# Kernel tuning notes

Measured on AMD Instinct MI355X. Metric: run time of the kernel, lower is better.

Reference implementation:

```python
import jax, jax.numpy as jnp
import numpy as np

N, E, D, L = 40000, 640000, 128, 4

def setup_inputs() -> dict:
    key = jax.random.key(0)
    ks = jax.random.split(key, 4)
    x = jax.random.normal(ks[0], (N, D), dtype=jnp.float32)
    edge_index = jax.random.randint(ks[1], (2, E), 0, N)
    edge_weight = jax.random.uniform(ks[2], (E,), dtype=jnp.float32)
    W = jax.random.normal(ks[3], (L, D, D), dtype=jnp.float32) / np.float32(np.sqrt(D))
    b = jnp.zeros((L, D), jnp.float32)
    gamma = jnp.ones((L, D), jnp.float32)
    beta = jnp.zeros((L, D), jnp.float32)
    return dict(x=x, edge_index=edge_index, edge_weight=edge_weight, W=W, b=b, gamma=gamma, beta=beta)

def _gcn_norm(edge_index, edge_weight, n):
    # PyG gcn_norm: add self loops (weight 1), symmetric D^-1/2 A D^-1/2
    loops = jnp.arange(n)
    src = jnp.concatenate([edge_index[0], loops])
    dst = jnp.concatenate([edge_index[1], loops])
    ew = jnp.concatenate([edge_weight, jnp.ones((n,), edge_weight.dtype)])
    deg = jax.ops.segment_sum(ew, dst, num_segments=n)
    dis = jnp.where(deg > 0, jax.lax.rsqrt(jnp.maximum(deg, 1e-12)), 0.0)
    return src, dst, dis[src] * ew * dis[dst]

def _batchnorm(h, g, bta):
    # training-mode BatchNorm1d over the node axis, biased variance, eps=1e-5
    mu = h.mean(0)
    var = h.var(0)
    return g * (h - mu) * jax.lax.rsqrt(var + 1e-5) + bta

def reference(x, edge_index, edge_weight, W, b, gamma, beta):
    n = x.shape[0]
    n_layers = W.shape[0]
    src, dst, norm = _gcn_norm(edge_index, edge_weight, n)
    x0 = x  # decoded_reshaped_x for skip connections
    for i in range(n_layers):
        h = x @ W[i]                                   # [N, D] linear (GCNConv.lin)
        msg = h[src] * norm[:, None]                   # gather + scale, [E+N, D]
        h = jax.ops.segment_sum(msg, dst, num_segments=n) + b[i]
        if i < n_layers - 1:
            h = jax.nn.relu(h)
        h = h + x0                                     # skip connection
        if i != n_layers - 2:
            h = _batchnorm(h, gamma[i], beta[i])
        x = h
    return x
```

## Files before the change

### kernel.cpp

```cpp
#include <hip/hip_runtime.h>
#include <cstdint>
#include <cstddef>

constexpr int N = 40000;
constexpr int E = 640000;
constexpr int D = 128;
constexpr int NBKT = 157;
constexpr int BCAP = 5120;
constexpr int AGG_GRID = 2500;

typedef _Float16 half8 __attribute__((ext_vector_type(8)));
typedef float f32x4 __attribute__((ext_vector_type(4)));
typedef unsigned long long ull;

__device__ __forceinline__ unsigned int pack_rec(int idx, float v) {
  union { _Float16 h; unsigned short us; } c; c.h = (_Float16)v;
  return (unsigned int)idx | ((unsigned int)c.us << 16);
}


__global__ void k_zero(uint4* __restrict__ p) {
  int i = blockIdx.x * 256 + threadIdx.x;
  if (i < 2136) p[i] = make_uint4(0u, 0u, 0u, 0u);
}


__global__ void k_bigprep(const int* __restrict__ ei, const float* __restrict__ ew,
                          const float* __restrict__ X, _Float16* __restrict__ Xh,
                          const float* __restrict__ W, _Float16* __restrict__ Wt,
                          ull* __restrict__ binned, int* __restrict__ bktcnt) {
  int bid = blockIdx.x, t = threadIdx.x;
  if (bid < NBKT) {
    __shared__ int lhist[NBKT], lbase[NBKT], lrank[NBKT];
    if (t < NBKT) { lhist[t] = 0; lrank[t] = 0; }
    __syncthreads();
    int e16 = bid * 256 + t;
    bool act = (e16 < E / 16);
    int4 s4[4], d4[4]; float4 w4[4];
    if (act) {
#pragma unroll
      for (int u = 0; u < 4; ++u) {
        s4[u] = ((const int4*)ei)[e16 * 4 + u];
        d4[u] = ((const int4*)(ei + E))[e16 * 4 + u];
        w4[u] = ((const float4*)ew)[e16 * 4 + u];
      }
#pragma unroll
      for (int u = 0; u < 4; ++u) {
        atomicAdd(&lhist[d4[u].x >> 8], 1); atomicAdd(&lhist[d4[u].y >> 8], 1);
        atomicAdd(&lhist[d4[u].z >> 8], 1); atomicAdd(&lhist[d4[u].w >> 8], 1);
      }
    }
    __syncthreads();
    if (t < NBKT && lhist[t] > 0) lbase[t] = atomicAdd(&bktcnt[t], lhist[t]);
    __syncthreads();
    if (act) {
      auto emit = [&](int s, int dcol, float w) {
        int bkt = dcol >> 8;
        int rank = atomicAdd(&lrank[bkt], 1);
        int pos = lbase[bkt] + rank;
        ull rec = (ull)(unsigned)(s & 0xFFFF)
                | ((ull)(unsigned)(dcol & 255) << 16)
                | ((ull)__float2uint_rn(w * 67108864.0f) << 24);
        if (pos < BCAP) binned[(size_t)bkt * BCAP + pos] = rec;
      };
#pragma unroll
      for (int u = 0; u < 4; ++u) {
        emit(s4[u].x, d4[u].x, w4[u].x); emit(s4[u].y, d4[u].y, w4[u].y);
        emit(s4[u].z, d4[u].z, w4[u].z); emit(s4[u].w, d4[u].w, w4[u].w);
      }
    }
  } else if (bid < 2657) {
    int i = (bid - NBKT) * 256 + t;
    float4 v0 = ((const float4*)X)[i * 2];
    float4 v1 = ((const float4*)X)[i * 2 + 1];
    half8 h;
    h[0] = (_Float16)v0.x; h[1] = (_Float16)v0.y; h[2] = (_Float16)v0.z; h[3] = (_Float16)v0.w;
    h[4] = (_Float16)v1.x; h[5] = (_Float16)v1.y; h[6] = (_Float16)v1.z; h[7] = (_Float16)v1.w;
    ((half8*)Xh)[i] = h;
  } else {
    int o = (bid - 2657) * 256 + t;
    int l = o >> 14, rem = o & 16383, c = rem >> 7, k = rem & 127;
    Wt[o] = (_Float16)W[l * 16384 + k * 128 + c];
  }
}


__global__ __launch_bounds__(256) void k_bstats(const ull* __restrict__ binned,
    const int* __restrict__ bktcnt, float* __restrict__ dis, int* __restrict__ rowc,
    int* __restrict__ bsum, int* __restrict__ hist, int* __restrict__ bpre,
    int* __restrict__ histcur, unsigned int* __restrict__ done) {
  __shared__ ull acc[256];
  __shared__ int lhist[64];
  __shared__ int red[256];
  __shared__ int amlast;
  int bkt = blockIdx.x, t = threadIdx.x;
  acc[t] = 0ULL;
  if (t < 64) lhist[t] = 0;
  __syncthreads();
  int cnt = min(bktcnt[bkt], BCAP);
  const ull* bp = binned + (size_t)bkt * BCAP;
  for (int e = t; e < cnt; e += 256) {
    ull r = bp[e];
    int local = (int)((r >> 16) & 255);
    atomicAdd(&acc[local], (1ULL << 40) | (r >> 24));
  }
  __syncthreads();
  int row = bkt * 256 + t;
  int c = 0;
  if (row < N) {
    ull a = acc[t];
    c = (int)(a >> 40) + 1;
    float deg = (float)(a & ((1ULL << 40) - 1)) * (1.0f / 67108864.0f);
    dis[row] = rsqrtf(deg + 1.0f);
    rowc[row] = c;
    atomicAdd(&lhist[min(c, 63)], 1);
  }
  red[t] = c;
  __syncthreads();
  for (int off = 128; off > 0; off >>= 1) {
    if (t < off) red[t] += red[t + off];
    __syncthreads();
  }
  if (t == 0) bsum[bkt] = red[0];
  if (t < 64 && lhist[t] > 0) atomicAdd(&hist[t], lhist[t]);
  __syncthreads();
  if (t == 0) {
    __threadfence();
    amlast = (atomicAdd(done, 1u) == NBKT - 1);
  }
  __syncthreads();
  if (!amlast) return;
  __threadfence();
  red[t] = (t < NBKT) ? bsum[t] : 0;
  __syncthreads();
  for (int off = 1; off < 256; off <<= 1) {
    int v = red[t];
    int add = (t >= off) ? red[t - off] : 0;
    __syncthreads();
    red[t] = v + add;
    __syncthreads();
  }
  if (t < NBKT) bpre[t] = (t == 0) ? 0 : red[t - 1];
  if (t < 64) {
    int s = 0;
    for (int b2 = t + 1; b2 < 64; ++b2) s += hist[b2];
    histcur[t] = s;
  }
}


__device__ __forceinline__ void gemm_body(int bid, int tid, const _Float16* __restrict__ X,
    const _Float16* __restrict__ Wt, const float* __restrict__ sums,
    const float* __restrict__ gamma, const float* __restrict__ beta, int useBN,
    const float* __restrict__ dis, _Float16* __restrict__ Hout,
    float* scl, float* shf) {
  if (tid < 128) {
    if (useBN) {
      float s = 0.f, s2 = 0.f;
#pragma unroll
      for (int r = 0; r < 8; ++r) { s += sums[r * 256 + tid]; s2 += sums[r * 256 + 128 + tid]; }
      float mu = s * (1.0f / N);
      float var = s2 * (1.0f / N) - mu * mu;
      float rs = rsqrtf(var + 1e-5f);
      float sc = gamma[tid] * rs;
      scl[tid] = sc;
      shf[tid] = beta[tid] - mu * sc;
    } else {
      scl[tid] = 1.0f;
      shf[tid] = 0.0f;
    }
  }
  __syncthreads();

  int wv = tid >> 6, lane = tid & 63;
  int fr = lane & 15, kg = lane >> 4;
  int arow = bid * 64 + wv * 16 + fr;
  const _Float16* xrow = X + (size_t)arow * D;

  half8 af[4];
#pragma unroll
  for (int kc = 0; kc < 4; ++kc) {
    int k0 = kc * 32 + kg * 8;
    half8 xr = *(const half8*)&xrow[k0];
    half8 a;
#pragma unroll
    for (int u = 0; u < 8; ++u)
      a[u] = (_Float16)fmaf((float)xr[u], scl[k0 + u], shf[k0 + u]);
    af[kc] = a;
  }

  f32x4 acc[8];
#pragma unroll
  for (int ct = 0; ct < 8; ++ct) acc[ct] = (f32x4){0.f, 0.f, 0.f, 0.f};

#pragma unroll
  for (int ct = 0; ct < 8; ++ct) {
    const _Float16* wcol = Wt + (size_t)(ct * 16 + fr) * 128;
#pragma unroll
    for (int kc = 0; kc < 4; ++kc) {
      half8 bf = *(const half8*)&wcol[kc * 32 + kg * 8];
      acc[ct] = __builtin_amdgcn_mfma_f32_16x16x32_f16(af[kc], bf, acc[ct], 0, 0, 0);
    }
  }

  int orow0 = bid * 64 + wv * 16 + kg * 4;
#pragma unroll
  for (int rg = 0; rg < 4; ++rg) {
    int grow = orow0 + rg;
    float dsv = dis[grow];
    _Float16* hrow = Hout + (size_t)grow * D;
#pragma unroll
    for (int ct = 0; ct < 8; ++ct)
      hrow[ct * 16 + fr] = (_Float16)(acc[ct][rg] * dsv);
  }
}

__global__ __launch_bounds__(256) void k_gemm(const _Float16* __restrict__ X,
    const _Float16* __restrict__ Wt, const float* __restrict__ sums,
    const float* __restrict__ gamma, const float* __restrict__ beta, int useBN,
    const float* __restrict__ dis, _Float16* __restrict__ Hout) {
  __shared__ float scl[128], shf[128];
  gemm_body(blockIdx.x, threadIdx.x, X, Wt, sums, gamma, beta, useBN, dis, Hout, scl, shf);
}


__global__ __launch_bounds__(256) void k_gemm0_fill(const _Float16* __restrict__ X,
    const _Float16* __restrict__ Wt, const float* __restrict__ dis,
    _Float16* __restrict__ Hout,
    const int* __restrict__ rowc, const int* __restrict__ bpre,
    const ull* __restrict__ binned, const int* __restrict__ bktcnt,
    unsigned int* __restrict__ cv, int* __restrict__ offs,
    int* __restrict__ histcur, int* __restrict__ perm) {
  int bid = blockIdx.x, t = threadIdx.x;
  if (bid < 625) {
    __shared__ float scl[128], shf[128];
    gemm_body(bid, t, X, Wt, (const float*)nullptr, (const float*)nullptr,
              (const float*)nullptr, 0, dis, Hout, scl, shf);
  } else if (bid < 625 + NBKT) {
    int bkt = bid - 625;
    __shared__ int lcur[256];
    __shared__ int s[256];
    int row = bkt * 256 + t;
    int c = (row < N) ? rowc[row] : 0;
    s[t] = c;
    __syncthreads();
    for (int off = 1; off < 256; off <<= 1) {
      int v = s[t];
      int add = (t >= off) ? s[t - off] : 0;
      __syncthreads();
      s[t] = v + add;
      __syncthreads();
    }
    int run = bpre[bkt] + s[t] - c;
    if (row < N) {
      offs[row] = run;
      cv[run] = pack_rec(row, 1.0f);
      lcur[t] = run + 1;
    } else {
      lcur[t] = 0;
    }
    if (row == N - 1) offs[N] = N + E;
    __syncthreads();
    int cnt = min(bktcnt[bkt], BCAP);
    const ull* bp = binned + (size_t)bkt * BCAP;
    for (int e = t; e < cnt; e += 256) {
      ull r = bp[e];
      int local = (int)((r >> 16) & 255);
      int srcv = (int)(r & 0xFFFFu);
      float w = (float)(unsigned)(r >> 24) * (1.0f / 67108864.0f);
      int slot = atomicAdd(&lcur[local], 1);
      cv[slot] = pack_rec(srcv, w);
    }
  } else {
    __shared__ int lhist[64], lbase[64];
    if (t < 64) lhist[t] = 0;
    __syncthreads();
    int i = (bid - (625 + NBKT)) * 256 + t;
    bool valid = (i < N);
    int bin = 0, myrank = 0;
    if (valid) {
      int c = rowc[i];
      bin = min(c, 63);
      myrank = atomicAdd(&lhist[bin], 1);
    }
    __syncthreads();
    if (t < 64 && lhist[t] > 0) lbase[t] = atomicAdd(&histcur[t], lhist[t]);
    __syncthreads();
    if (valid) perm[lbase[bin] + myrank] = i;
  }
}


__global__ __launch_bounds__(256) void k_agg(const uint4* __restrict__ Hu4,
    const int* __restrict__ offs, const unsigned int* __restrict__ cv,
    const float* __restrict__ dis, const float* __restrict__ bias,
    const uint4* __restrict__ x0h, const int* __restrict__ perm,
    int doRelu, int doStats, int outF32,
    _Float16* __restrict__ Hout16, float* __restrict__ Houtf, float* __restrict__ sums) {
  int t = threadIdx.x;
  int sl = t & 15;
  int g = t >> 4;
  int row = perm[blockIdx.x * 16 + g];
  float4 bv0 = ((const float4*)bias)[sl * 2];
  float4 bv1 = ((const float4*)bias)[sl * 2 + 1];
  const uint4* hp = Hu4 + sl;

  int e0 = offs[row], e1 = offs[row + 1];
  float a[8];
#pragma unroll
  for (int k = 0; k < 8; ++k) a[k] = 0.f;
  for (int eb = e0; eb < e1; eb += 16) {
    int m = min(16, e1 - eb);
    unsigned int rec = 0;
    if (sl < m) rec = cv[eb + sl];
#pragma unroll 1
    for (int g8 = 0; g8 < 2; ++g8) {
      int b0 = g8 * 8;
      if (b0 >= m) break;
      uint4 cu[8]; float vv[8];
#pragma unroll
      for (int j = 0; j < 8; ++j) {
        int jj = b0 + j;
        int jc = (jj < m) ? jj : (m - 1);
        unsigned int rj = __shfl(rec, jc, 16);
        union { unsigned short us; _Float16 h; } vh; vh.us = (unsigned short)(rj >> 16);
        vv[j] = (jj < m) ? (float)vh.h : 0.f;
        cu[j] = hp[(size_t)(rj & 0xFFFFu) * 16];
      }
#pragma unroll
      for (int j = 0; j < 8; ++j) {
        union { uint4 u; _Float16 hh[8]; } c8; c8.u = cu[j];
#pragma unroll
        for (int k = 0; k < 8; ++k) a[k] = fmaf((float)c8.hh[k], vv[j], a[k]);
      }
    }
  }
  float dr = dis[row];
  union { uint4 u; _Float16 hh[8]; } xc;
  xc.u = x0h[(size_t)row * 16 + sl];
  float rr[8];
  rr[0] = fmaf(a[0], dr, bv0.x); rr[1] = fmaf(a[1], dr, bv0.y);
  rr[2] = fmaf(a[2], dr, bv0.z); rr[3] = fmaf(a[3], dr, bv0.w);
  rr[4] = fmaf(a[4], dr, bv1.x); rr[5] = fmaf(a[5], dr, bv1.y);
  rr[6] = fmaf(a[6], dr, bv1.z); rr[7] = fmaf(a[7], dr, bv1.w);
  if (doRelu) {
#pragma unroll
    for (int k = 0; k < 8; ++k) rr[k] = fmaxf(rr[k], 0.f);
  }
#pragma unroll
  for (int k = 0; k < 8; ++k) rr[k] += (float)xc.hh[k];
  if (outF32) {
    float4 o0, o1;
    o0.x = rr[0]; o0.y = rr[1]; o0.z = rr[2]; o0.w = rr[3];
    o1.x = rr[4]; o1.y = rr[5]; o1.z = rr[6]; o1.w = rr[7];
    ((float4*)Houtf)[(size_t)row * 32 + sl * 2] = o0;
    ((float4*)Houtf)[(size_t)row * 32 + sl * 2 + 1] = o1;
  } else {
    union { uint4 u; _Float16 hh[8]; } ov;
#pragma unroll
    for (int k = 0; k < 8; ++k) ov.hh[k] = (_Float16)rr[k];
    ((uint4*)Hout16)[(size_t)row * 16 + sl] = ov.u;
  }

  if (doStats) {
    __shared__ float reds[16 * 128], reds2[16 * 128];
#pragma unroll
    for (int k = 0; k < 8; ++k) {
      reds[g * 128 + sl * 8 + k] = rr[k];
      reds2[g * 128 + sl * 8 + k] = rr[k] * rr[k];
    }
    __syncthreads();
    if (t < 128) {
      float ts = 0.f, ts2 = 0.f;
#pragma unroll
      for (int j = 0; j < 16; ++j) { ts += reds[j * 128 + t]; ts2 += reds2[j * 128 + t]; }
      int rep = blockIdx.x & 7;
      atomicAdd(&sums[rep * 256 + t], ts);
      atomicAdd(&sums[rep * 256 + 128 + t], ts2);
    }
  }
}


__global__ __launch_bounds__(256) void k_bnapply(float* __restrict__ H,
    const float* __restrict__ sums, const float* __restrict__ gamma,
    const float* __restrict__ beta) {
  __shared__ float scl[128], shf[128];
  int t = threadIdx.x;
  if (t < 128) {
    float s = 0.f, s2 = 0.f;
#pragma unroll
    for (int r = 0; r < 8; ++r) { s += sums[r * 256 + t]; s2 += sums[r * 256 + 128 + t]; }
    float mu = s * (1.0f / N);
    float var = s2 * (1.0f / N) - mu * mu;
    float rs = rsqrtf(var + 1e-5f);
    float sc = gamma[t] * rs;
    scl[t] = sc;
    shf[t] = beta[t] - mu * sc;
  }
  __syncthreads();
  size_t i = (size_t)blockIdx.x * 256 + t;
  float4 v = ((const float4*)H)[i];
  int c = (int)(i & 31) * 4;
  v.x = fmaf(v.x, scl[c + 0], shf[c + 0]);
  v.y = fmaf(v.y, scl[c + 1], shf[c + 1]);
  v.z = fmaf(v.z, scl[c + 2], shf[c + 2]);
  v.w = fmaf(v.w, scl[c + 3], shf[c + 3]);
  ((float4*)H)[i] = v;
}


extern "C" void kernel_launch(void* const* d_in, const int* in_sizes, int n_in,
                              void* d_out, int out_size, void* d_ws, size_t ws_size,
                              hipStream_t stream) {
  const float* x     = (const float*)d_in[0];
  const int*   ei    = (const int*)d_in[1];
  const float* ew    = (const float*)d_in[2];
  const float* W     = (const float*)d_in[3];
  const float* b     = (const float*)d_in[4];
  const float* gamma = (const float*)d_in[5];
  const float* beta  = (const float*)d_in[6];
  float* out = (float*)d_out;

  char* ws = (char*)d_ws;
  _Float16* hlin   = (_Float16*)ws;
  _Float16* hagg16 = (_Float16*)(ws + 10240000);
  _Float16* xh     = (_Float16*)(ws + 20480000);
  float* sums4    = (float*)(ws + 30720000);
  int*   hist     = (int*)  (ws + 30752768);
  int*   histcur  = (int*)  (ws + 30753024);
  int*   bktcnt   = (int*)  (ws + 30753280);
  unsigned int* done = (unsigned int*)(ws + 30753920);
  float* dis      = (float*)(ws + 30754176);
  int*   offs     = (int*)  (ws + 30914176);
  int*   rowc     = (int*)  (ws + 31074192);
  unsigned int* cv= (unsigned int*)(ws + 31234192);
  int*   perm     = (int*)  (ws + 33954192);
  int*   bsum     = (int*)  (ws + 34114192);
  int*   bpre     = (int*)  (ws + 34114832);
  _Float16* Wt    = (_Float16*)(ws + 34115472);
  ull* binned     = (ull*)  (ws + 34246544);

  k_zero<<<9, 256, 0, stream>>>((uint4*)sums4);
  k_bigprep<<<2913, 256, 0, stream>>>(ei, ew, x, xh, W, Wt, binned, bktcnt);
  k_bstats<<<NBKT, 256, 0, stream>>>(binned, bktcnt, dis, rowc, bsum, hist,
                                     bpre, histcur, done);

  for (int l = 0; l < 4; ++l) {
    const _Float16* xin = (l == 0) ? xh : hagg16;
    if (l == 0) {
      k_gemm0_fill<<<625 + NBKT + 157, 256, 0, stream>>>(xin, Wt, dis, hlin,
                                                         rowc, bpre, binned, bktcnt,
                                                         cv, offs, histcur, perm);
    } else {
      int useBN = (l == 1 || l == 2) ? 1 : 0;
      const float* sprev = sums4 + (size_t)(l - 1) * 2048;
      k_gemm<<<N / 64, 256, 0, stream>>>(xin, Wt + (size_t)l * 16384, sprev,
                                         gamma + (size_t)(l - 1) * D,
                                         beta + (size_t)(l - 1) * D, useBN, dis, hlin);
    }
    int doStats = (l != 2) ? 1 : 0;
    int doRelu = (l < 3) ? 1 : 0;
    int outF32 = (l == 3) ? 1 : 0;
    k_agg<<<AGG_GRID, 256, 0, stream>>>((const uint4*)hlin, offs, cv, dis,
                                        b + (size_t)l * D, (const uint4*)xh, perm,
                                        doRelu, doStats, outF32, hagg16, out,
                                        sums4 + (size_t)l * 2048);
  }
  k_bnapply<<<(N * D / 4) / 256, 256, 0, stream>>>(out, sums4 + 3 * 2048,
                                                   gamma + 3 * D, beta + 3 * D);
}
```

Baseline: 230.5 us.

## Slice feature columns into four planes so aggregation gathers stay cache-resident

Stores the fp16 node features as four column slices of 32 channels each, with the GEMM reading and writing that sliced layout. The aggregation kernel runs four times as many blocks, one set per slice, and each thread gathers a 4-byte pair instead of a 16-byte chunk. The aim is to shrink the working set of each gather pass (40000×32 fp16 per slice) so random neighbour reads hit in L2 or infinity cache. In exchange, CSR edge records are re-read once per slice, each gather moves less data, and nontemporal hints are added on the streaming loads and stores.

```diff
diff --git a/kernel.cpp b/kernel.cpp
--- a/kernel.cpp
+++ b/kernel.cpp
@@ -8,9 +8,15 @@
 constexpr int NBKT = 157;
 constexpr int BCAP = 5120;
 constexpr int AGG_GRID = 2500;
+constexpr int NSLICE = 4;
+constexpr size_t SLICE_H  = (size_t)N * 32;
+constexpr size_t SLICE_D  = (size_t)N * 16;
+constexpr size_t SLICE_H8 = (size_t)N * 4;
 
 typedef _Float16 half8 __attribute__((ext_vector_type(8)));
+typedef _Float16 half2v __attribute__((ext_vector_type(2)));
 typedef float f32x4 __attribute__((ext_vector_type(4)));
+typedef float f32x2 __attribute__((ext_vector_type(2)));
 typedef unsigned long long ull;
 
 __device__ __forceinline__ unsigned int pack_rec(int idx, float v) {
@@ -76,7 +82,8 @@
     half8 h;
     h[0] = (_Float16)v0.x; h[1] = (_Float16)v0.y; h[2] = (_Float16)v0.z; h[3] = (_Float16)v0.w;
     h[4] = (_Float16)v1.x; h[5] = (_Float16)v1.y; h[6] = (_Float16)v1.z; h[7] = (_Float16)v1.w;
-    ((half8*)Xh)[i] = h;
+    int r = i >> 4, c8 = i & 15;
+    ((half8*)Xh)[(size_t)(c8 >> 2) * SLICE_H8 + (size_t)r * 4 + (c8 & 3)] = h;
   } else {
     int o = (bid - 2657) * 256 + t;
     int l = o >> 14, rem = o & 16383, c = rem >> 7, k = rem & 127;
@@ -175,13 +182,12 @@
   int wv = tid >> 6, lane = tid & 63;
   int fr = lane & 15, kg = lane >> 4;
   int arow = bid * 64 + wv * 16 + fr;
-  const _Float16* xrow = X + (size_t)arow * D;
 
   half8 af[4];
 #pragma unroll
   for (int kc = 0; kc < 4; ++kc) {
     int k0 = kc * 32 + kg * 8;
-    half8 xr = *(const half8*)&xrow[k0];
+    half8 xr = *(const half8*)&X[(size_t)kc * SLICE_H + (size_t)arow * 32 + kg * 8];
     half8 a;
 #pragma unroll
     for (int u = 0; u < 8; ++u)
@@ -208,10 +214,11 @@
   for (int rg = 0; rg < 4; ++rg) {
     int grow = orow0 + rg;
     float dsv = dis[grow];
-    _Float16* hrow = Hout + (size_t)grow * D;
-#pragma unroll
-    for (int ct = 0; ct < 8; ++ct)
-      hrow[ct * 16 + fr] = (_Float16)(acc[ct][rg] * dsv);
+#pragma unroll
+    for (int ct = 0; ct < 8; ++ct) {
+      Hout[(size_t)(ct >> 1) * SLICE_H + (size_t)grow * 32 + (ct & 1) * 16 + fr] =
+          (_Float16)(acc[ct][rg] * dsv);
+    }
   }
 }
 
@@ -291,92 +298,72 @@
 }
 
 
-__global__ __launch_bounds__(256) void k_agg(const uint4* __restrict__ Hu4,
+__global__ __launch_bounds__(256) void k_agg(const unsigned int* __restrict__ Hu,
     const int* __restrict__ offs, const unsigned int* __restrict__ cv,
     const float* __restrict__ dis, const float* __restrict__ bias,
-    const uint4* __restrict__ x0h, const int* __restrict__ perm,
+    const unsigned int* __restrict__ x0u, const int* __restrict__ perm,
     int doRelu, int doStats, int outF32,
-    _Float16* __restrict__ Hout16, float* __restrict__ Houtf, float* __restrict__ sums) {
+    unsigned int* __restrict__ Hout16, float* __restrict__ Houtf,
+    float* __restrict__ sums) {
   int t = threadIdx.x;
+  int blk = blockIdx.x % AGG_GRID;
+  int slice = blockIdx.x / AGG_GRID;
   int sl = t & 15;
   int g = t >> 4;
-  int row = perm[blockIdx.x * 16 + g];
-  float4 bv0 = ((const float4*)bias)[sl * 2];
-  float4 bv1 = ((const float4*)bias)[sl * 2 + 1];
-  const uint4* hp = Hu4 + sl;
+  int row = perm[blk * 16 + g];
+  int C0 = slice * 32;
+  float bvx = bias[C0 + sl * 2];
+  float bvy = bias[C0 + sl * 2 + 1];
+  const unsigned int* hb = Hu + (size_t)slice * SLICE_D + sl;
 
   int e0 = offs[row], e1 = offs[row + 1];
-  float a[8];
-#pragma unroll
-  for (int k = 0; k < 8; ++k) a[k] = 0.f;
+  float a0 = 0.f, a1 = 0.f;
   for (int eb = e0; eb < e1; eb += 16) {
     int m = min(16, e1 - eb);
     unsigned int rec = 0;
-    if (sl < m) rec = cv[eb + sl];
-#pragma unroll 1
-    for (int g8 = 0; g8 < 2; ++g8) {
-      int b0 = g8 * 8;
-      if (b0 >= m) break;
-      uint4 cu[8]; float vv[8];
-#pragma unroll
-      for (int j = 0; j < 8; ++j) {
-        int jj = b0 + j;
-        int jc = (jj < m) ? jj : (m - 1);
-        unsigned int rj = __shfl(rec, jc, 16);
-        union { unsigned short us; _Float16 h; } vh; vh.us = (unsigned short)(rj >> 16);
-        vv[j] = (jj < m) ? (float)vh.h : 0.f;
-        cu[j] = hp[(size_t)(rj & 0xFFFFu) * 16];
-      }
-#pragma unroll
-      for (int j = 0; j < 8; ++j) {
-        union { uint4 u; _Float16 hh[8]; } c8; c8.u = cu[j];
-#pragma unroll
-        for (int k = 0; k < 8; ++k) a[k] = fmaf((float)c8.hh[k], vv[j], a[k]);
-      }
+    if (sl < m) rec = __builtin_nontemporal_load(&cv[eb + sl]);
+#pragma unroll 4
+    for (int j = 0; j < m; ++j) {
+      unsigned int rj = __shfl(rec, j, 16);
+      union { unsigned short us; _Float16 h; } vh; vh.us = (unsigned short)(rj >> 16);
+      float vj = (float)vh.h;
+      union { unsigned int u; half2v h; } hh;
+      hh.u = hb[(size_t)(rj & 0xFFFFu) * 16];
+      a0 = fmaf((float)hh.h[0], vj, a0);
+      a1 = fmaf((float)hh.h[1], vj, a1);
     }
   }
   float dr = dis[row];
-  union { uint4 u; _Float16 hh[8]; } xc;
-  xc.u = x0h[(size_t)row * 16 + sl];
-  float rr[8];
-  rr[0] = fmaf(a[0], dr, bv0.x); rr[1] = fmaf(a[1], dr, bv0.y);
-  rr[2] = fmaf(a[2], dr, bv0.z); rr[3] = fmaf(a[3], dr, bv0.w);
-  rr[4] = fmaf(a[4], dr, bv1.x); rr[5] = fmaf(a[5], dr, bv1.y);
-  rr[6] = fmaf(a[6], dr, bv1.z); rr[7] = fmaf(a[7], dr, bv1.w);
-  if (doRelu) {
-#pragma unroll
-    for (int k = 0; k < 8; ++k) rr[k] = fmaxf(rr[k], 0.f);
-  }
-#pragma unroll
-  for (int k = 0; k < 8; ++k) rr[k] += (float)xc.hh[k];
+  union { unsigned int u; half2v h; } xc;
+  xc.u = __builtin_nontemporal_load(&x0u[(size_t)slice * SLICE_D + (size_t)row * 16 + sl]);
+  float r0 = fmaf(a0, dr, bvx);
+  float r1 = fmaf(a1, dr, bvy);
+  if (doRelu) { r0 = fmaxf(r0, 0.f); r1 = fmaxf(r1, 0.f); }
+  r0 += (float)xc.h[0];
+  r1 += (float)xc.h[1];
   if (outF32) {
-    float4 o0, o1;
-    o0.x = rr[0]; o0.y = rr[1]; o0.z = rr[2]; o0.w = rr[3];
-    o1.x = rr[4]; o1.y = rr[5]; o1.z = rr[6]; o1.w = rr[7];
-    ((float4*)Houtf)[(size_t)row * 32 + sl * 2] = o0;
-    ((float4*)Houtf)[(size_t)row * 32 + sl * 2 + 1] = o1;
+    f32x2 o; o[0] = r0; o[1] = r1;
+    __builtin_nontemporal_store(o, (f32x2*)&Houtf[(size_t)row * 128 + C0 + sl * 2]);
   } else {
-    union { uint4 u; _Float16 hh[8]; } ov;
-#pragma unroll
-    for (int k = 0; k < 8; ++k) ov.hh[k] = (_Float16)rr[k];
-    ((uint4*)Hout16)[(size_t)row * 16 + sl] = ov.u;
+    union { unsigned int u; half2v h; } ov;
+    ov.h[0] = (_Float16)r0; ov.h[1] = (_Float16)r1;
+    Hout16[(size_t)slice * SLICE_D + (size_t)row * 16 + sl] = ov.u;
   }
 
   if (doStats) {
-    __shared__ float reds[16 * 128], reds2[16 * 128];
-#pragma unroll
-    for (int k = 0; k < 8; ++k) {
-      reds[g * 128 + sl * 8 + k] = rr[k];
-      reds2[g * 128 + sl * 8 + k] = rr[k] * rr[k];
-    }
-    __syncthreads();
-    if (t < 128) {
+    __shared__ float reds[512], reds2[512];
+    reds[g * 32 + sl * 2]      = r0;
+    reds[g * 32 + sl * 2 + 1]  = r1;
+    reds2[g * 32 + sl * 2]     = r0 * r0;
+    reds2[g * 32 + sl * 2 + 1] = r1 * r1;
+    __syncthreads();
+    if (t < 32) {
       float ts = 0.f, ts2 = 0.f;
 #pragma unroll
-      for (int j = 0; j < 16; ++j) { ts += reds[j * 128 + t]; ts2 += reds2[j * 128 + t]; }
-      int rep = blockIdx.x & 7;
-      atomicAdd(&sums[rep * 256 + t], ts);
-      atomicAdd(&sums[rep * 256 + 128 + t], ts2);
+      for (int q = 0; q < 16; ++q) { ts += reds[q * 32 + t]; ts2 += reds2[q * 32 + t]; }
+      int rep = blk & 7;
+      atomicAdd(&sums[rep * 256 + C0 + t], ts);
+      atomicAdd(&sums[rep * 256 + 128 + C0 + t], ts2);
     }
   }
 }
@@ -462,9 +449,11 @@
     int doStats = (l != 2) ? 1 : 0;
     int doRelu = (l < 3) ? 1 : 0;
     int outF32 = (l == 3) ? 1 : 0;
-    k_agg<<<AGG_GRID, 256, 0, stream>>>((const uint4*)hlin, offs, cv, dis,
-                                        b + (size_t)l * D, (const uint4*)xh, perm,
-                                        doRelu, doStats, outF32, hagg16, out,
+    k_agg<<<NSLICE * AGG_GRID, 256, 0, stream>>>((const unsigned int*)hlin, offs, cv,
+                                        dis, b + (size_t)l * D,
+                                        (const unsigned int*)xh, perm,
+                                        doRelu, doStats, outF32,
+                                        (unsigned int*)hagg16, out,
                                         sums4 + (size_t)l * 2048);
   }
   k_bnapply<<<(N * D / 4) / 256, 256, 0, stream>>>(out, sums4 + 3 * 2048,
```

Measured after the change: 342.5 us. 1.49x slower.

## Group each row's CSR edges by source-node tile and restructure gather loop

Applied to the files above, without the earlier changes.

Edges in each destination row are now ordered by one of four source-index tiles, with per-row tile counts packed into a 64-bit word built in the stats kernel and used by the fill kernel to lay out four sub-ranges per row. The aggregation kernel walks the tiles in order, aiming to improve L2 locality of the feature-row gathers. The gather loop also changes from batching eight independent loads before the FMAs to a simple per-edge load-and-accumulate loop, which may reduce memory-level parallelism. The extra tile counters add shared-memory atomics in preprocessing.

```diff
diff --git a/kernel.cpp b/kernel.cpp
--- a/kernel.cpp
+++ b/kernel.cpp
@@ -16,6 +16,10 @@
 __device__ __forceinline__ unsigned int pack_rec(int idx, float v) {
   union { _Float16 h; unsigned short us; } c; c.h = (_Float16)v;
   return (unsigned int)idx | ((unsigned int)c.us << 16);
+}
+
+__device__ __forceinline__ int src_tile(int s) {
+  return (int)(((unsigned)s * 6711u) >> 26);
 }
 
 
@@ -87,14 +91,17 @@
 
 __global__ __launch_bounds__(256) void k_bstats(const ull* __restrict__ binned,
     const int* __restrict__ bktcnt, float* __restrict__ dis, int* __restrict__ rowc,
+    ull* __restrict__ tilecnt,
     int* __restrict__ bsum, int* __restrict__ hist, int* __restrict__ bpre,
     int* __restrict__ histcur, unsigned int* __restrict__ done) {
   __shared__ ull acc[256];
+  __shared__ ull cnt4[256];
   __shared__ int lhist[64];
   __shared__ int red[256];
   __shared__ int amlast;
   int bkt = blockIdx.x, t = threadIdx.x;
   acc[t] = 0ULL;
+  cnt4[t] = 0ULL;
   if (t < 64) lhist[t] = 0;
   __syncthreads();
   int cnt = min(bktcnt[bkt], BCAP);
@@ -102,7 +109,9 @@
   for (int e = t; e < cnt; e += 256) {
     ull r = bp[e];
     int local = (int)((r >> 16) & 255);
+    int src = (int)(r & 0xFFFFu);
     atomicAdd(&acc[local], (1ULL << 40) | (r >> 24));
+    atomicAdd(&cnt4[local], 1ULL << (16 * src_tile(src)));
   }
   __syncthreads();
   int row = bkt * 256 + t;
@@ -113,6 +122,7 @@
     float deg = (float)(a & ((1ULL << 40) - 1)) * (1.0f / 67108864.0f);
     dis[row] = rsqrtf(deg + 1.0f);
     rowc[row] = c;
+    tilecnt[row] = cnt4[t] + (1ULL << (16 * src_tile(row)));
     atomicAdd(&lhist[min(c, 63)], 1);
   }
   red[t] = c;
@@ -227,7 +237,8 @@
 __global__ __launch_bounds__(256) void k_gemm0_fill(const _Float16* __restrict__ X,
     const _Float16* __restrict__ Wt, const float* __restrict__ dis,
     _Float16* __restrict__ Hout,
-    const int* __restrict__ rowc, const int* __restrict__ bpre,
+    const int* __restrict__ rowc, const ull* __restrict__ tilecnt,
+    const int* __restrict__ bpre,
     const ull* __restrict__ binned, const int* __restrict__ bktcnt,
     unsigned int* __restrict__ cv, int* __restrict__ offs,
     int* __restrict__ histcur, int* __restrict__ perm) {
@@ -238,7 +249,7 @@
               (const float*)nullptr, 0, dis, Hout, scl, shf);
   } else if (bid < 625 + NBKT) {
     int bkt = bid - 625;
-    __shared__ int lcur[256];
+    __shared__ int lcur[256 * 4];
     __shared__ int s[256];
     int row = bkt * 256 + t;
     int c = (row < N) ? rowc[row] : 0;
@@ -254,10 +265,20 @@
     int run = bpre[bkt] + s[t] - c;
     if (row < N) {
       offs[row] = run;
-      cv[run] = pack_rec(row, 1.0f);
-      lcur[t] = run + 1;
+      ull tc = tilecnt[row];
+      int b0 = run;
+      int b1 = b0 + (int)(tc & 0xFFFF);
+      int b2 = b1 + (int)((tc >> 16) & 0xFFFF);
+      int b3 = b2 + (int)((tc >> 32) & 0xFFFF);
+      lcur[t * 4 + 0] = b0; lcur[t * 4 + 1] = b1;
+      lcur[t * 4 + 2] = b2; lcur[t * 4 + 3] = b3;
+      int ts = src_tile(row);
+      int slot = lcur[t * 4 + ts];
+      cv[slot] = pack_rec(row, 1.0f);
+      lcur[t * 4 + ts] = slot + 1;
     } else {
-      lcur[t] = 0;
+#pragma unroll
+      for (int k = 0; k < 4; ++k) lcur[t * 4 + k] = 0;
     }
     if (row == N - 1) offs[N] = N + E;
     __syncthreads();
@@ -268,7 +289,7 @@
       int local = (int)((r >> 16) & 255);
       int srcv = (int)(r & 0xFFFFu);
       float w = (float)(unsigned)(r >> 24) * (1.0f / 67108864.0f);
-      int slot = atomicAdd(&lcur[local], 1);
+      int slot = atomicAdd(&lcur[local * 4 + src_tile(srcv)], 1);
       cv[slot] = pack_rec(srcv, w);
     }
   } else {
@@ -292,7 +313,8 @@
 
 
 __global__ __launch_bounds__(256) void k_agg(const uint4* __restrict__ Hu4,
-    const int* __restrict__ offs, const unsigned int* __restrict__ cv,
+    const int* __restrict__ offs, const ull* __restrict__ tilecnt,
+    const unsigned int* __restrict__ cv,
     const float* __restrict__ dis, const float* __restrict__ bias,
     const uint4* __restrict__ x0h, const int* __restrict__ perm,
     int doRelu, int doStats, int outF32,
@@ -305,35 +327,32 @@
   float4 bv1 = ((const float4*)bias)[sl * 2 + 1];
   const uint4* hp = Hu4 + sl;
 
-  int e0 = offs[row], e1 = offs[row + 1];
+  ull tc = tilecnt[row];
+  int e = offs[row];
   float a[8];
 #pragma unroll
   for (int k = 0; k < 8; ++k) a[k] = 0.f;
-  for (int eb = e0; eb < e1; eb += 16) {
-    int m = min(16, e1 - eb);
-    unsigned int rec = 0;
-    if (sl < m) rec = cv[eb + sl];
 #pragma unroll 1
-    for (int g8 = 0; g8 < 2; ++g8) {
-      int b0 = g8 * 8;
-      if (b0 >= m) break;
-      uint4 cu[8]; float vv[8];
-#pragma unroll
-      for (int j = 0; j < 8; ++j) {
-        int jj = b0 + j;
-        int jc = (jj < m) ? jj : (m - 1);
-        unsigned int rj = __shfl(rec, jc, 16);
+  for (int tile = 0; tile < 4; ++tile) {
+    int cnt = (int)((tc >> (16 * tile)) & 0xFFFF);
+    int eend = e + cnt;
+    for (int eb = e; eb < eend; eb += 16) {
+      int m = min(16, eend - eb);
+      unsigned int rec = 0;
+      if (sl < m) rec = cv[eb + sl];
+#pragma unroll 8
+      for (int j = 0; j < m; ++j) {
+        unsigned int rj = __shfl(rec, j, 16);
+        int sj = (int)(rj & 0xFFFFu);
         union { unsigned short us; _Float16 h; } vh; vh.us = (unsigned short)(rj >> 16);
-        vv[j] = (jj < m) ? (float)vh.h : 0.f;
-        cu[j] = hp[(size_t)(rj & 0xFFFFu) * 16];
+        float vj = (float)vh.h;
+        union { uint4 u; _Float16 hh[8]; } cu;
+        cu.u = hp[(size_t)sj * 16];
+#pragma unroll
+        for (int k = 0; k < 8; ++k) a[k] = fmaf((float)cu.hh[k], vj, a[k]);
       }
-#pragma unroll
-      for (int j = 0; j < 8; ++j) {
-        union { uint4 u; _Float16 hh[8]; } c8; c8.u = cu[j];
-#pragma unroll
-        for (int k = 0; k < 8; ++k) a[k] = fmaf((float)c8.hh[k], vv[j], a[k]);
-      }
-    }
+    }
+    e = eend;
   }
   float dr = dis[row];
   union { uint4 u; _Float16 hh[8]; } xc;
@@ -373,7 +392,7 @@
     if (t < 128) {
       float ts = 0.f, ts2 = 0.f;
 #pragma unroll
-      for (int j = 0; j < 16; ++j) { ts += reds[j * 128 + t]; ts2 += reds2[j * 128 + t]; }
+      for (int j2 = 0; j2 < 16; ++j2) { ts += reds[j2 * 128 + t]; ts2 += reds2[j2 * 128 + t]; }
       int rep = blockIdx.x & 7;
       atomicAdd(&sums[rep * 256 + t], ts);
       atomicAdd(&sums[rep * 256 + 128 + t], ts2);
@@ -440,17 +459,19 @@
   int*   bpre     = (int*)  (ws + 34114832);
   _Float16* Wt    = (_Float16*)(ws + 34115472);
   ull* binned     = (ull*)  (ws + 34246544);
+  ull* tilecnt    = (ull*)  (ws + 40677264);
 
   k_zero<<<9, 256, 0, stream>>>((uint4*)sums4);
   k_bigprep<<<2913, 256, 0, stream>>>(ei, ew, x, xh, W, Wt, binned, bktcnt);
-  k_bstats<<<NBKT, 256, 0, stream>>>(binned, bktcnt, dis, rowc, bsum, hist,
-                                     bpre, histcur, done);
+  k_bstats<<<NBKT, 256, 0, stream>>>(binned, bktcnt, dis, rowc, tilecnt,
+                                     bsum, hist, bpre, histcur, done);
 
   for (int l = 0; l < 4; ++l) {
     const _Float16* xin = (l == 0) ? xh : hagg16;
     if (l == 0) {
       k_gemm0_fill<<<625 + NBKT + 157, 256, 0, stream>>>(xin, Wt, dis, hlin,
-                                                         rowc, bpre, binned, bktcnt,
+                                                         rowc, tilecnt, bpre,
+                                                         binned, bktcnt,
                                                          cv, offs, histcur, perm);
     } else {
       int useBN = (l == 1 || l == 2) ? 1 : 0;
@@ -462,7 +483,7 @@
     int doStats = (l != 2) ? 1 : 0;
     int doRelu = (l < 3) ? 1 : 0;
     int outF32 = (l == 3) ? 1 : 0;
-    k_agg<<<AGG_GRID, 256, 0, stream>>>((const uint4*)hlin, offs, cv, dis,
+    k_agg<<<AGG_GRID, 256, 0, stream>>>((const uint4*)hlin, offs, tilecnt, cv, dis,
                                         b + (size_t)l * D, (const uint4*)xh, perm,
                                         doRelu, doStats, outF32, hagg16, out,
                                         sums4 + (size_t)l * 2048);
```

Result: slower. 246.5 us (+7.0%).
